# Kernel tuning notes

Hardware: AMD Instinct MI355X
Metric: run time of the kernel (lower is better)

## Reference

```python
import jax, jax.numpy as jnp
import numpy as np
import math

B, T, D, H, E = 4, 2048, 1024, 4096, 8
CAPACITY_FACTOR = 1.0
MIN_CAPACITY = 4
Z_LOSS_COEF = 0.001
AUX_LOSS_COEF = 0.01


def setup_inputs() -> dict:
    key = jax.random.key(0)
    ks = jax.random.split(key, 5)
    x = jax.random.normal(ks[0], (B, T, D), jnp.float32)
    Wg = jax.random.normal(ks[1], (D, E), jnp.float32) * 0.02
    W1 = jax.random.normal(ks[2], (E, D, H), jnp.float32) * (1.0 / math.sqrt(D))
    b1 = jnp.zeros((E, H), jnp.float32)
    W2 = jax.random.normal(ks[3], (E, H, D), jnp.float32) * (1.0 / math.sqrt(H))
    b2 = jnp.zeros((E, D), jnp.float32)
    return {"x": x, "Wg": Wg, "W1": W1, "b1": b1, "W2": W2, "b2": b2}


def reference(x, Wg, W1, b1, W2, b2):
    b, t, d = x.shape
    e = Wg.shape[1]
    N = b * t
    capacity = max(MIN_CAPACITY, math.ceil(CAPACITY_FACTOR * N / e))  # static
    xf = x.reshape(N, d)

    # ---- Router (top-1, z-loss + aux load-balancing loss) ----
    logits = xf @ Wg                                   # [N, E]
    probs = jax.nn.softmax(logits, axis=-1)
    z_loss = jnp.mean(jax.nn.logsumexp(logits, axis=-1) ** 2)
    expert_index = jnp.argmax(logits, axis=-1)         # [N]
    expert_prob = jnp.take_along_axis(probs, expert_index[:, None], axis=1)[:, 0]
    counts = jax.ops.segment_sum(jnp.ones((N,), jnp.float32), expert_index,
                                 num_segments=e)       # bincount
    f_i = counts / N
    p_i = probs.mean(axis=0)
    aux_loss = AUX_LOSS_COEF * e * jnp.sum(f_i * p_i) + Z_LOSS_COEF * z_loss

    # ---- Sort-based dispatch ----
    sort_idx = jnp.argsort(expert_index)               # stable sort by expert
    se = expert_index[sort_idx]                        # sorted expert ids
    xs = xf[sort_idx]                                  # tokens in sorted order
    ps = expert_prob[sort_idx]                         # probs in sorted order
    counts_i = counts.astype(jnp.int32)
    start = jnp.cumsum(counts_i) - counts_i            # per-expert start offsets
    pos = jnp.arange(N, dtype=jnp.int32) - start[se]   # slot within expert
    keep = pos < capacity                              # capacity drop
    slot = jnp.where(keep, pos, capacity)              # overflow -> trash slot

    # Gather tokens into per-expert capacity buffer [E, capacity+1, D]
    buf = jnp.zeros((e, capacity + 1, d), xf.dtype).at[se, slot].set(xs)

    # ---- Batched per-expert MLP (grouped GEMM) ----
    h = jax.nn.gelu(jnp.einsum('ecd,edh->ech', buf, W1) + b1[:, None, :],
                    approximate=False)
    o = jnp.einsum('ech,ehd->ecd', h, W2) + b2[:, None, :]

    # ---- Combine: gather back, zero dropped tokens, unsort ----
    out_sorted = jnp.where(keep[:, None], o[se, slot], jnp.zeros((), o.dtype))
    out = jnp.zeros_like(xf).at[sort_idx].set(out_sorted)
    # NOTE: faithful to original code, which multiplies the UNSORTED output by
    # the SORTED probabilities (prob_sorted), a quirk of the source module.
    out = out * ps[:, None]
    return out.reshape(b, t, d), aux_loss
```

## Files before the change

kernel.cpp:

```cpp
#include <hip/hip_runtime.h>
#include <math.h>

#define N_TOK 8192
#define DIM   1024
#define NEXP  8
#define HID   4096
#define CAP   1024
#define TPT   (N_TOK / 256)
#define RT_BLOCKS 1024
#define RT_TPB 8

typedef _Float16 f16x8 __attribute__((ext_vector_type(8)));
typedef _Float16 f16x4 __attribute__((ext_vector_type(4)));
typedef float    f32x4 __attribute__((ext_vector_type(4)));

__device__ __forceinline__ float gelu_fast(float v) {
    const float v2 = v * v;
    const float u = v * (0.79788456f + 0.035677408136f * v2);
    const float ex = __expf(2.f * u);
    const float th = 1.f - 2.f / (1.f + ex);
    return 0.5f * v * (1.f + th);
}

__device__ __forceinline__ void gl_lds16(const void* g, void* l) {
    __builtin_amdgcn_global_load_lds(
        (const __attribute__((address_space(1))) unsigned int*)g,
        (__attribute__((address_space(3))) unsigned int*)l, 16, 0, 0);
}

__global__ __launch_bounds__(256) void router_kernel(
    const float* __restrict__ x, const float* __restrict__ Wg,
    int* __restrict__ ei, float* __restrict__ eprob,
    float* __restrict__ pp)
{
    __shared__ float psum_s[NEXP + 1];
    const int tid = threadIdx.x;
    const int w = tid >> 6, lane = tid & 63;
    if (tid <= NEXP) psum_s[tid] = 0.f;
    __syncthreads();

    float p_loc[NEXP];
#pragma unroll
    for (int e = 0; e < NEXP; ++e) p_loc[e] = 0.f;
    float z_loc = 0.f;

#pragma unroll
    for (int ti = 0; ti < 2; ++ti) {
        const int t = blockIdx.x * RT_TPB + w * 2 + ti;
        const float* xr = x + (size_t)t * DIM;
        float acc[NEXP];
#pragma unroll
        for (int e = 0; e < NEXP; ++e) acc[e] = 0.f;
#pragma unroll
        for (int k = 0; k < DIM / 256; ++k) {
            const int d = k * 256 + lane * 4;
            const float4 xv = *(const float4*)(xr + d);
            const float xs[4] = {xv.x, xv.y, xv.z, xv.w};
#pragma unroll
            for (int u = 0; u < 4; ++u) {
                const float4 w0 = *(const float4*)(Wg + (size_t)(d + u) * NEXP);
                const float4 w1 = *(const float4*)(Wg + (size_t)(d + u) * NEXP + 4);
                acc[0] += xs[u] * w0.x; acc[1] += xs[u] * w0.y;
                acc[2] += xs[u] * w0.z; acc[3] += xs[u] * w0.w;
                acc[4] += xs[u] * w1.x; acc[5] += xs[u] * w1.y;
                acc[6] += xs[u] * w1.z; acc[7] += xs[u] * w1.w;
            }
        }
#pragma unroll
        for (int off = 32; off > 0; off >>= 1) {
#pragma unroll
            for (int e = 0; e < NEXP; ++e)
                acc[e] += __shfl_down(acc[e], off, 64);
        }
        if (lane == 0) {
            float m = acc[0]; int arg = 0;
#pragma unroll
            for (int e = 1; e < NEXP; ++e) { if (acc[e] > m) { m = acc[e]; arg = e; } }
            float ex[NEXP]; float se = 0.f;
#pragma unroll
            for (int e = 0; e < NEXP; ++e) { ex[e] = expf(acc[e] - m); se += ex[e]; }
            const float lse = m + logf(se);
            const float inv = 1.f / se;
#pragma unroll
            for (int e = 0; e < NEXP; ++e) p_loc[e] += ex[e] * inv;
            z_loc += lse * lse;
            ei[t] = arg;
            eprob[t] = ex[arg] * inv;
        }
    }
    if (lane == 0) {
#pragma unroll
        for (int e = 0; e < NEXP; ++e) atomicAdd(&psum_s[e], p_loc[e]);
        atomicAdd(&psum_s[NEXP], z_loc);
    }
    __syncthreads();
    if (tid <= NEXP) pp[blockIdx.x * (NEXP + 1) + tid] = psum_s[tid];
}

__global__ __launch_bounds__(256) void dispatch_kernel(
    const int* __restrict__ ei, const float* __restrict__ eprob,
    int* __restrict__ slot_to_token, int* __restrict__ sort_idx,
    float* __restrict__ scale,
    const float* __restrict__ pp,
    int* __restrict__ dropped, int* __restrict__ n_dropped,
    float* __restrict__ aux_out)
{
    __shared__ int hist[NEXP][256];
    __shared__ int start_s[NEXP];
    __shared__ float red_s[4][NEXP + 1];
    __shared__ float tot_s[NEXP + 1];
    __shared__ int ndrop_s;
    const int t = threadIdx.x;
    const int w = t >> 6, lane = t & 63;
    if (t == 0) ndrop_s = 0;

    {
        float v[NEXP + 1];
#pragma unroll
        for (int j = 0; j <= NEXP; ++j) v[j] = 0.f;
        for (int g = 0; g < RT_BLOCKS / 256; ++g)
#pragma unroll
            for (int j = 0; j <= NEXP; ++j) v[j] += pp[(size_t)(g * 256 + t) * (NEXP + 1) + j];
#pragma unroll
        for (int j = 0; j <= NEXP; ++j) {
            float s = v[j];
#pragma unroll
            for (int off = 32; off > 0; off >>= 1) s += __shfl_down(s, off, 64);
            if (lane == 0) red_s[w][j] = s;
        }
    }
    __syncthreads();
    if (t <= NEXP) tot_s[t] = red_s[0][t] + red_s[1][t] + red_s[2][t] + red_s[3][t];
    __syncthreads();

    int le[TPT];
    int lh[NEXP];
#pragma unroll
    for (int e = 0; e < NEXP; ++e) lh[e] = 0;
    const int base = t * TPT;
    for (int i = 0; i < TPT; ++i) {
        const int e = ei[base + i];
        le[i] = e;
        lh[e]++;
    }
#pragma unroll
    for (int e = 0; e < NEXP; ++e) hist[e][t] = lh[e];
    __syncthreads();
    for (int off = 1; off < 256; off <<= 1) {
        int v[NEXP];
#pragma unroll
        for (int e = 0; e < NEXP; ++e) v[e] = (t >= off) ? hist[e][t - off] : 0;
        __syncthreads();
#pragma unroll
        for (int e = 0; e < NEXP; ++e) hist[e][t] += v[e];
        __syncthreads();
    }
    if (t == 0) {
        int s = 0;
        for (int e = 0; e < NEXP; ++e) { start_s[e] = s; s += hist[e][255]; }
    }
    __syncthreads();
    int run[NEXP];
#pragma unroll
    for (int e = 0; e < NEXP; ++e) run[e] = (t > 0) ? hist[e][t - 1] : 0;
    for (int i = 0; i < TPT; ++i) {
        const int n = base + i;
        const int e = le[i];
        const int pos = run[e]++;
        sort_idx[start_s[e] + pos] = n;
        if (pos < CAP) {
            slot_to_token[e * CAP + pos] = n;
        } else {
            const int di = atomicAdd(&ndrop_s, 1);
            dropped[di] = n;
        }
    }
    __syncthreads();
    for (int n = t; n < N_TOK; n += 256) scale[n] = eprob[sort_idx[n]];
    if (t == 0) {
        n_dropped[0] = ndrop_s;
        float s = 0.f;
        for (int e = 0; e < NEXP; ++e) {
            const float f = (float)hist[e][255] / (float)N_TOK;
            const float p = tot_s[e] / (float)N_TOK;
            s += f * p;
        }
        aux_out[0] = 0.01f * (float)NEXP * s + 0.001f * (tot_s[NEXP] / (float)N_TOK);
    }
}

__global__ __launch_bounds__(256) void zero_dropped_kernel(
    const int* __restrict__ dropped, const int* __restrict__ n_dropped,
    float* __restrict__ out)
{
    const int nd = n_dropped[0];
    const float4 z = make_float4(0.f, 0.f, 0.f, 0.f);
    for (int idx = blockIdx.x; idx < nd; idx += gridDim.x) {
        const int tok = dropped[idx];
        *(float4*)(out + (size_t)tok * DIM + threadIdx.x * 4) = z;
    }
}

__global__ __launch_bounds__(256) void gather_kernel(
    const float* __restrict__ x, const int* __restrict__ slot_to_token,
    _Float16* __restrict__ Xbuf)
{
    const int slot = blockIdx.x;
    const int tok = slot_to_token[slot];
    const int c = threadIdx.x * 4;
    float4 v = make_float4(0.f, 0.f, 0.f, 0.f);
    if (tok >= 0) v = *(const float4*)(x + (size_t)tok * DIM + c);
    f16x4 o;
    o[0] = (_Float16)v.x; o[1] = (_Float16)v.y;
    o[2] = (_Float16)v.z; o[3] = (_Float16)v.w;
    *(f16x4*)(Xbuf + (size_t)slot * DIM + c) = o;
}

template<int R, int C>
__global__ __launch_bounds__(256) void transpose_f32_f16(
    const float* __restrict__ in, _Float16* __restrict__ outT)
{
    const int e = blockIdx.z;
    const int r0 = blockIdx.y * 64, c0 = blockIdx.x * 64;
    const float* pin = in + (size_t)e * R * C;
    _Float16* pot = outT + (size_t)e * R * C;
    __shared__ _Float16 tile[64][72];
    const int tid = threadIdx.x;
    const int rr = tid >> 4, cc = (tid & 15) * 4;
#pragma unroll
    for (int ri = 0; ri < 4; ++ri) {
        const int row = rr + ri * 16;
        const float4 v = *(const float4*)&pin[(size_t)(r0 + row) * C + c0 + cc];
        tile[cc + 0][row] = (_Float16)v.x;
        tile[cc + 1][row] = (_Float16)v.y;
        tile[cc + 2][row] = (_Float16)v.z;
        tile[cc + 3][row] = (_Float16)v.w;
    }
    __syncthreads();
    const int c = tid >> 2, rs = (tid & 3) * 16;
    const f16x8 o0 = *(const f16x8*)&tile[c][rs];
    const f16x8 o1 = *(const f16x8*)&tile[c][rs + 8];
    _Float16* po = &pot[(size_t)(c0 + c) * R + r0 + rs];
    *(f16x8*)po = o0;
    *(f16x8*)(po + 8) = o1;
}

__global__ __launch_bounds__(256) void gemm1_kernel(
    const _Float16* __restrict__ A, const _Float16* __restrict__ Bt,
    const float* __restrict__ b1, _Float16* __restrict__ Hbuf)
{
    const int b = blockIdx.x;
    const int xcd = b & 7, q = b >> 3;
    const int nb = (xcd << 2) | (q & 3);
    const int mb = q >> 2;
    const int e  = mb >> 3;
    const _Float16* Ab = A  + (size_t)mb * 128 * DIM;
    const _Float16* Bb = Bt + (size_t)e * HID * DIM + (size_t)nb * 128 * DIM;
    __shared__ _Float16 As[128 * 32];
    __shared__ _Float16 Bs[128 * 32];
    const int tid = threadIdx.x;
    const int lane = tid & 63, w = tid >> 6;
    const int wm = (w >> 1) * 64, wn = (w & 1) * 64;
    const int lr = lane & 15, quad = lane >> 4;

    f32x4 acc[4][4];
#pragma unroll
    for (int i = 0; i < 4; ++i)
#pragma unroll
        for (int j = 0; j < 4; ++j) acc[i][j] = (f32x4)0.f;

    for (int k0 = 0; k0 < DIM; k0 += 32) {
#pragma unroll
        for (int i = 0; i < 2; ++i) {
            const int idx = i * 256 + tid;
            const int row = idx >> 2, s = idx & 3;
            const int seg = s ^ (row & 3);
            gl_lds16(Ab + (size_t)row * DIM + k0 + seg * 8, &As[idx * 8]);
            gl_lds16(Bb + (size_t)row * DIM + k0 + seg * 8, &Bs[idx * 8]);
        }
        __syncthreads();
        f16x8 af[4], bf[4];
#pragma unroll
        for (int i = 0; i < 4; ++i) {
            const int R = wm + i * 16 + lr;
            af[i] = *(const f16x8*)&As[R * 32 + (quad ^ (R & 3)) * 8];
        }
#pragma unroll
        for (int j = 0; j < 4; ++j) {
            const int R = wn + j * 16 + lr;
            bf[j] = *(const f16x8*)&Bs[R * 32 + (quad ^ (R & 3)) * 8];
        }
#pragma unroll
        for (int i = 0; i < 4; ++i)
#pragma unroll
            for (int j = 0; j < 4; ++j)
                acc[i][j] = __builtin_amdgcn_mfma_f32_16x16x32_f16(af[i], bf[j], acc[i][j], 0, 0, 0);
        __syncthreads();
    }
    float bias[4];
#pragma unroll
    for (int j = 0; j < 4; ++j)
        bias[j] = b1[(size_t)e * HID + (size_t)nb * 128 + wn + j * 16 + lr];
#pragma unroll
    for (int i = 0; i < 4; ++i) {
#pragma unroll
        for (int r = 0; r < 4; ++r) {
            const size_t row = (size_t)mb * 128 + wm + i * 16 + quad * 4 + r;
            _Float16* hr = Hbuf + row * HID + (size_t)nb * 128;
#pragma unroll
            for (int j = 0; j < 4; ++j)
                hr[wn + j * 16 + lr] = (_Float16)gelu_fast(acc[i][j][r] + bias[j]);
        }
    }
}

__global__ __launch_bounds__(256) void gemm2_kernel(
    const _Float16* __restrict__ A, const _Float16* __restrict__ Bt,
    const float* __restrict__ b2, const int* __restrict__ slot_to_token,
    const float* __restrict__ scale, float* __restrict__ out)
{
    const int mb = blockIdx.x;
    const int nb = blockIdx.y;
    const int e  = mb >> 3;
    const _Float16* Ab = A  + (size_t)mb * 128 * HID;
    const _Float16* Bb = Bt + (size_t)e * DIM * HID + (size_t)nb * 128 * HID;
    __shared__ _Float16 As[128 * 32];
    __shared__ _Float16 Bs[128 * 32];
    const int tid = threadIdx.x;
    const int lane = tid & 63, w = tid >> 6;
    const int wm = (w >> 1) * 64, wn = (w & 1) * 64;
    const int lr = lane & 15, quad = lane >> 4;

    f32x4 acc[4][4];
#pragma unroll
    for (int i = 0; i < 4; ++i)
#pragma unroll
        for (int j = 0; j < 4; ++j) acc[i][j] = (f32x4)0.f;

    for (int k0 = 0; k0 < HID; k0 += 32) {
#pragma unroll
        for (int i = 0; i < 2; ++i) {
            const int idx = i * 256 + tid;
            const int row = idx >> 2, s = idx & 3;
            const int seg = s ^ (row & 3);
            gl_lds16(Ab + (size_t)row * HID + k0 + seg * 8, &As[idx * 8]);
            gl_lds16(Bb + (size_t)row * HID + k0 + seg * 8, &Bs[idx * 8]);
        }
        __syncthreads();
        f16x8 af[4], bf[4];
#pragma unroll
        for (int i = 0; i < 4; ++i) {
            const int R = wm + i * 16 + lr;
            af[i] = *(const f16x8*)&As[R * 32 + (quad ^ (R & 3)) * 8];
        }
#pragma unroll
        for (int j = 0; j < 4; ++j) {
            const int R = wn + j * 16 + lr;
            bf[j] = *(const f16x8*)&Bs[R * 32 + (quad ^ (R & 3)) * 8];
        }
#pragma unroll
        for (int i = 0; i < 4; ++i)
#pragma unroll
            for (int j = 0; j < 4; ++j)
                acc[i][j] = __builtin_amdgcn_mfma_f32_16x16x32_f16(af[i], bf[j], acc[i][j], 0, 0, 0);
        __syncthreads();
    }
    float bias[4];
#pragma unroll
    for (int j = 0; j < 4; ++j)
        bias[j] = b2[(size_t)e * DIM + (size_t)nb * 128 + wn + j * 16 + lr];
#pragma unroll
    for (int i = 0; i < 4; ++i) {
#pragma unroll
        for (int r = 0; r < 4; ++r) {
            const int slot = mb * 128 + wm + i * 16 + quad * 4 + r;
            const int tok = slot_to_token[slot];
            if (tok >= 0) {
                const float sc = scale[tok];
                float* orow = out + (size_t)tok * DIM + (size_t)nb * 128;
#pragma unroll
                for (int j = 0; j < 4; ++j)
                    orow[wn + j * 16 + lr] = (acc[i][j][r] + bias[j]) * sc;
            }
        }
    }
}

extern "C" void kernel_launch(void* const* d_in, const int* in_sizes, int n_in,
                              void* d_out, int out_size, void* d_ws, size_t ws_size,
                              hipStream_t stream)
{
    const float* x  = (const float*)d_in[0];
    const float* Wg = (const float*)d_in[1];
    const float* W1 = (const float*)d_in[2];
    const float* b1 = (const float*)d_in[3];
    const float* W2 = (const float*)d_in[4];
    const float* b2 = (const float*)d_in[5];
    float* out = (float*)d_out;

    _Float16* Wt   = (_Float16*)d_ws;
    _Float16* Xbuf = Wt + (size_t)NEXP * HID * DIM;
    _Float16* Hbuf = Xbuf + (size_t)N_TOK * DIM;
    int*   ei    = (int*)(Hbuf + (size_t)N_TOK * HID);
    float* eprob = (float*)(ei + N_TOK);
    int*   sort_idx = (int*)(eprob + N_TOK);
    float* scale = (float*)(sort_idx + N_TOK);
    int*   s2t   = (int*)(scale + N_TOK);
    float* pp    = (float*)(s2t + NEXP * CAP);
    int*   dropped = (int*)(pp + RT_BLOCKS * (NEXP + 1));
    int*   n_dropped = dropped + N_TOK;

    hipMemsetAsync(s2t, 0xFF, (size_t)NEXP * CAP * sizeof(int), stream);

    transpose_f32_f16<DIM, HID><<<dim3(HID / 64, DIM / 64, NEXP), 256, 0, stream>>>(W1, Wt);
    router_kernel<<<RT_BLOCKS, 256, 0, stream>>>(x, Wg, ei, eprob, pp);
    dispatch_kernel<<<1, 256, 0, stream>>>(ei, eprob, s2t, sort_idx, scale,
                                           pp, dropped, n_dropped,
                                           out + (size_t)N_TOK * DIM);
    zero_dropped_kernel<<<128, 256, 0, stream>>>(dropped, n_dropped, out);
    gather_kernel<<<NEXP * CAP, 256, 0, stream>>>(x, s2t, Xbuf);
    gemm1_kernel<<<2048, 256, 0, stream>>>(Xbuf, Wt, b1, Hbuf);
    transpose_f32_f16<HID, DIM><<<dim3(DIM / 64, HID / 64, NEXP), 256, 0, stream>>>(W2, Wt);
    gemm2_kernel<<<dim3(64, 8), 256, 0, stream>>>(Hbuf, Wt, b2, s2t, scale, out);
}
```

Baseline: 590.0 us.

## Triple-buffer MoE grouped GEMMs with 256x128 tiles and XCD-aware expert mapping

```diff
diff --git a/kernel.cpp b/kernel.cpp
--- a/kernel.cpp
+++ b/kernel.cpp
@@ -245,142 +245,215 @@
     *(f16x8*)(po + 8) = o1;
 }
 
-__global__ __launch_bounds__(256) void gemm1_kernel(
+
+__global__ __launch_bounds__(256, 2) void gemm1_kernel(
     const _Float16* __restrict__ A, const _Float16* __restrict__ Bt,
     const float* __restrict__ b1, _Float16* __restrict__ Hbuf)
 {
     const int b = blockIdx.x;
     const int xcd = b & 7, q = b >> 3;
-    const int nb = (xcd << 2) | (q & 3);
-    const int mb = q >> 2;
-    const int e  = mb >> 3;
-    const _Float16* Ab = A  + (size_t)mb * 128 * DIM;
+    const int mbl = q & 3, nb = q >> 2;
+    const int e = xcd, mb = (xcd << 2) | mbl;
+    const _Float16* Ab = A  + (size_t)mb * 256 * DIM;
     const _Float16* Bb = Bt + (size_t)e * HID * DIM + (size_t)nb * 128 * DIM;
-    __shared__ _Float16 As[128 * 32];
-    __shared__ _Float16 Bs[128 * 32];
+    __shared__ _Float16 As[3][256 * 32];
+    __shared__ _Float16 Bs[3][128 * 32];
     const int tid = threadIdx.x;
     const int lane = tid & 63, w = tid >> 6;
-    const int wm = (w >> 1) * 64, wn = (w & 1) * 64;
+    const int wr = w >> 1, wc = w & 1;
     const int lr = lane & 15, quad = lane >> 4;
-
-    f32x4 acc[4][4];
-#pragma unroll
-    for (int i = 0; i < 4; ++i)
-#pragma unroll
-        for (int j = 0; j < 4; ++j) acc[i][j] = (f32x4)0.f;
-
-    for (int k0 = 0; k0 < DIM; k0 += 32) {
+    const int rb = wr * 128, cb = wc * 64;
+
+    auto stage = [&](int t, int buf) {
+#pragma unroll
+        for (int i = 0; i < 4; ++i) {
+            const int idx = i * 256 + tid;
+            const int row = idx >> 2, s = idx & 3;
+            const int seg = s ^ ((row >> 1) & 3);
+            gl_lds16(Ab + (size_t)row * DIM + t * 32 + seg * 8, &As[buf][idx * 8]);
+        }
 #pragma unroll
         for (int i = 0; i < 2; ++i) {
             const int idx = i * 256 + tid;
             const int row = idx >> 2, s = idx & 3;
-            const int seg = s ^ (row & 3);
-            gl_lds16(Ab + (size_t)row * DIM + k0 + seg * 8, &As[idx * 8]);
-            gl_lds16(Bb + (size_t)row * DIM + k0 + seg * 8, &Bs[idx * 8]);
-        }
-        __syncthreads();
-        f16x8 af[4], bf[4];
-#pragma unroll
-        for (int i = 0; i < 4; ++i) {
-            const int R = wm + i * 16 + lr;
-            af[i] = *(const f16x8*)&As[R * 32 + (quad ^ (R & 3)) * 8];
-        }
-#pragma unroll
-        for (int j = 0; j < 4; ++j) {
-            const int R = wn + j * 16 + lr;
-            bf[j] = *(const f16x8*)&Bs[R * 32 + (quad ^ (R & 3)) * 8];
-        }
-#pragma unroll
-        for (int i = 0; i < 4; ++i)
-#pragma unroll
-            for (int j = 0; j < 4; ++j)
-                acc[i][j] = __builtin_amdgcn_mfma_f32_16x16x32_f16(af[i], bf[j], acc[i][j], 0, 0, 0);
-        __syncthreads();
-    }
+            const int seg = s ^ ((row >> 1) & 3);
+            gl_lds16(Bb + (size_t)row * DIM + t * 32 + seg * 8, &Bs[buf][idx * 8]);
+        }
+    };
+
+    f32x4 acc[8][4];
+#pragma unroll
+    for (int i = 0; i < 8; ++i)
+#pragma unroll
+        for (int j = 0; j < 4; ++j) acc[i][j] = (f32x4)0.f;
+
+    stage(0, 0);
+    stage(1, 1);
+    const int NT = DIM / 32;
+    int cur = 0;
+    for (int t = 0; t < NT; ++t) {
+        asm volatile("s_waitcnt vmcnt(6)" ::: "memory");
+        __builtin_amdgcn_s_barrier();
+        if (t + 2 < NT) {
+            int nx = cur + 2; if (nx >= 3) nx -= 3;
+            stage(t + 2, nx);
+        }
+        f16x8 af[8], bf[4];
+#pragma unroll
+        for (int m = 0; m < 4; ++m) {
+            const int R = rb + m * 16 + lr;
+            af[m] = *(const f16x8*)&As[cur][R * 32 + (quad ^ ((R >> 1) & 3)) * 8];
+        }
+#pragma unroll
+        for (int n = 0; n < 4; ++n) {
+            const int R = cb + n * 16 + lr;
+            bf[n] = *(const f16x8*)&Bs[cur][R * 32 + (quad ^ ((R >> 1) & 3)) * 8];
+        }
+        __builtin_amdgcn_s_barrier();
+        __builtin_amdgcn_s_setprio(1);
+#pragma unroll
+        for (int m = 0; m < 4; ++m)
+#pragma unroll
+            for (int n = 0; n < 4; ++n)
+                acc[m][n] = __builtin_amdgcn_mfma_f32_16x16x32_f16(af[m], bf[n], acc[m][n], 0, 0, 0);
+        __builtin_amdgcn_s_setprio(0);
+#pragma unroll
+        for (int m = 4; m < 8; ++m) {
+            const int R = rb + m * 16 + lr;
+            af[m] = *(const f16x8*)&As[cur][R * 32 + (quad ^ ((R >> 1) & 3)) * 8];
+        }
+        __builtin_amdgcn_s_setprio(1);
+#pragma unroll
+        for (int m = 4; m < 8; ++m)
+#pragma unroll
+            for (int n = 0; n < 4; ++n)
+                acc[m][n] = __builtin_amdgcn_mfma_f32_16x16x32_f16(af[m], bf[n], acc[m][n], 0, 0, 0);
+        __builtin_amdgcn_s_setprio(0);
+        cur = cur + 1; if (cur >= 3) cur -= 3;
+    }
+
+    const int colb = nb * 128 + cb;
     float bias[4];
 #pragma unroll
-    for (int j = 0; j < 4; ++j)
-        bias[j] = b1[(size_t)e * HID + (size_t)nb * 128 + wn + j * 16 + lr];
-#pragma unroll
-    for (int i = 0; i < 4; ++i) {
+    for (int n = 0; n < 4; ++n)
+        bias[n] = b1[(size_t)e * HID + colb + n * 16 + lr];
+#pragma unroll
+    for (int m = 0; m < 8; ++m) {
 #pragma unroll
         for (int r = 0; r < 4; ++r) {
-            const size_t row = (size_t)mb * 128 + wm + i * 16 + quad * 4 + r;
-            _Float16* hr = Hbuf + row * HID + (size_t)nb * 128;
-#pragma unroll
-            for (int j = 0; j < 4; ++j)
-                hr[wn + j * 16 + lr] = (_Float16)gelu_fast(acc[i][j][r] + bias[j]);
-        }
-    }
-}
-
-__global__ __launch_bounds__(256) void gemm2_kernel(
+            const size_t row = (size_t)mb * 256 + rb + m * 16 + quad * 4 + r;
+            _Float16* hr = Hbuf + row * HID + colb;
+#pragma unroll
+            for (int n = 0; n < 4; ++n)
+                hr[n * 16 + lr] = (_Float16)gelu_fast(acc[m][n][r] + bias[n]);
+        }
+    }
+}
+
+__global__ __launch_bounds__(256, 2) void gemm2_kernel(
     const _Float16* __restrict__ A, const _Float16* __restrict__ Bt,
     const float* __restrict__ b2, const int* __restrict__ slot_to_token,
     const float* __restrict__ scale, float* __restrict__ out)
 {
-    const int mb = blockIdx.x;
-    const int nb = blockIdx.y;
-    const int e  = mb >> 3;
-    const _Float16* Ab = A  + (size_t)mb * 128 * HID;
+    const int b = blockIdx.x;
+    const int xcd = b & 7, q = b >> 3;
+    const int mbl = q >> 3, nb = q & 7;
+    const int e = xcd, mb = (xcd << 2) | mbl;
+    const _Float16* Ab = A  + (size_t)mb * 256 * HID;
     const _Float16* Bb = Bt + (size_t)e * DIM * HID + (size_t)nb * 128 * HID;
-    __shared__ _Float16 As[128 * 32];
-    __shared__ _Float16 Bs[128 * 32];
+    __shared__ _Float16 As[3][256 * 32];
+    __shared__ _Float16 Bs[3][128 * 32];
     const int tid = threadIdx.x;
     const int lane = tid & 63, w = tid >> 6;
-    const int wm = (w >> 1) * 64, wn = (w & 1) * 64;
+    const int wr = w >> 1, wc = w & 1;
     const int lr = lane & 15, quad = lane >> 4;
-
-    f32x4 acc[4][4];
-#pragma unroll
-    for (int i = 0; i < 4; ++i)
-#pragma unroll
-        for (int j = 0; j < 4; ++j) acc[i][j] = (f32x4)0.f;
-
-    for (int k0 = 0; k0 < HID; k0 += 32) {
+    const int rb = wr * 128, cb = wc * 64;
+
+    auto stage = [&](int t, int buf) {
+#pragma unroll
+        for (int i = 0; i < 4; ++i) {
+            const int idx = i * 256 + tid;
+            const int row = idx >> 2, s = idx & 3;
+            const int seg = s ^ ((row >> 1) & 3);
+            gl_lds16(Ab + (size_t)row * HID + t * 32 + seg * 8, &As[buf][idx * 8]);
+        }
 #pragma unroll
         for (int i = 0; i < 2; ++i) {
             const int idx = i * 256 + tid;
             const int row = idx >> 2, s = idx & 3;
-            const int seg = s ^ (row & 3);
-            gl_lds16(Ab + (size_t)row * HID + k0 + seg * 8, &As[idx * 8]);
-            gl_lds16(Bb + (size_t)row * HID + k0 + seg * 8, &Bs[idx * 8]);
-        }
-        __syncthreads();
-        f16x8 af[4], bf[4];
-#pragma unroll
-        for (int i = 0; i < 4; ++i) {
-            const int R = wm + i * 16 + lr;
-            af[i] = *(const f16x8*)&As[R * 32 + (quad ^ (R & 3)) * 8];
-        }
-#pragma unroll
-        for (int j = 0; j < 4; ++j) {
-            const int R = wn + j * 16 + lr;
-            bf[j] = *(const f16x8*)&Bs[R * 32 + (quad ^ (R & 3)) * 8];
-        }
-#pragma unroll
-        for (int i = 0; i < 4; ++i)
-#pragma unroll
-            for (int j = 0; j < 4; ++j)
-                acc[i][j] = __builtin_amdgcn_mfma_f32_16x16x32_f16(af[i], bf[j], acc[i][j], 0, 0, 0);
-        __syncthreads();
-    }
+            const int seg = s ^ ((row >> 1) & 3);
+            gl_lds16(Bb + (size_t)row * HID + t * 32 + seg * 8, &Bs[buf][idx * 8]);
+        }
+    };
+
+    f32x4 acc[8][4];
+#pragma unroll
+    for (int i = 0; i < 8; ++i)
+#pragma unroll
+        for (int j = 0; j < 4; ++j) acc[i][j] = (f32x4)0.f;
+
+    stage(0, 0);
+    stage(1, 1);
+    const int NT = HID / 32;
+    int cur = 0;
+    for (int t = 0; t < NT; ++t) {
+        asm volatile("s_waitcnt vmcnt(6)" ::: "memory");
+        __builtin_amdgcn_s_barrier();
+        if (t + 2 < NT) {
+            int nx = cur + 2; if (nx >= 3) nx -= 3;
+            stage(t + 2, nx);
+        }
+        f16x8 af[8], bf[4];
+#pragma unroll
+        for (int m = 0; m < 4; ++m) {
+            const int R = rb + m * 16 + lr;
+            af[m] = *(const f16x8*)&As[cur][R * 32 + (quad ^ ((R >> 1) & 3)) * 8];
+        }
+#pragma unroll
+        for (int n = 0; n < 4; ++n) {
+            const int R = cb + n * 16 + lr;
+            bf[n] = *(const f16x8*)&Bs[cur][R * 32 + (quad ^ ((R >> 1) & 3)) * 8];
+        }
+        __builtin_amdgcn_s_barrier();
+        __builtin_amdgcn_s_setprio(1);
+#pragma unroll
+        for (int m = 0; m < 4; ++m)
+#pragma unroll
+            for (int n = 0; n < 4; ++n)
+                acc[m][n] = __builtin_amdgcn_mfma_f32_16x16x32_f16(af[m], bf[n], acc[m][n], 0, 0, 0);
+        __builtin_amdgcn_s_setprio(0);
+#pragma unroll
+        for (int m = 4; m < 8; ++m) {
+            const int R = rb + m * 16 + lr;
+            af[m] = *(const f16x8*)&As[cur][R * 32 + (quad ^ ((R >> 1) & 3)) * 8];
+        }
+        __builtin_amdgcn_s_setprio(1);
+#pragma unroll
+        for (int m = 4; m < 8; ++m)
+#pragma unroll
+            for (int n = 0; n < 4; ++n)
+                acc[m][n] = __builtin_amdgcn_mfma_f32_16x16x32_f16(af[m], bf[n], acc[m][n], 0, 0, 0);
+        __builtin_amdgcn_s_setprio(0);
+        cur = cur + 1; if (cur >= 3) cur -= 3;
+    }
+
+    const int colb = nb * 128 + cb;
     float bias[4];
 #pragma unroll
-    for (int j = 0; j < 4; ++j)
-        bias[j] = b2[(size_t)e * DIM + (size_t)nb * 128 + wn + j * 16 + lr];
-#pragma unroll
-    for (int i = 0; i < 4; ++i) {
+    for (int n = 0; n < 4; ++n)
+        bias[n] = b2[(size_t)e * DIM + colb + n * 16 + lr];
+#pragma unroll
+    for (int m = 0; m < 8; ++m) {
 #pragma unroll
         for (int r = 0; r < 4; ++r) {
-            const int slot = mb * 128 + wm + i * 16 + quad * 4 + r;
+            const int slot = mb * 256 + rb + m * 16 + quad * 4 + r;
             const int tok = slot_to_token[slot];
             if (tok >= 0) {
                 const float sc = scale[tok];
-                float* orow = out + (size_t)tok * DIM + (size_t)nb * 128;
-#pragma unroll
-                for (int j = 0; j < 4; ++j)
-                    orow[wn + j * 16 + lr] = (acc[i][j][r] + bias[j]) * sc;
+                float* orow = out + (size_t)tok * DIM + colb;
+#pragma unroll
+                for (int n = 0; n < 4; ++n)
+                    orow[n * 16 + lr] = (acc[m][n][r] + bias[n]) * sc;
             }
         }
     }
@@ -419,7 +492,7 @@
                                            out + (size_t)N_TOK * DIM);
     zero_dropped_kernel<<<128, 256, 0, stream>>>(dropped, n_dropped, out);
     gather_kernel<<<NEXP * CAP, 256, 0, stream>>>(x, s2t, Xbuf);
-    gemm1_kernel<<<2048, 256, 0, stream>>>(Xbuf, Wt, b1, Hbuf);
+    gemm1_kernel<<<1024, 256, 0, stream>>>(Xbuf, Wt, b1, Hbuf);
     transpose_f32_f16<HID, DIM><<<dim3(DIM / 64, HID / 64, NEXP), 256, 0, stream>>>(W2, Wt);
-    gemm2_kernel<<<dim3(64, 8), 256, 0, stream>>>(Hbuf, Wt, b2, s2t, scale, out);
-}
+    gemm2_kernel<<<256, 256, 0, stream>>>(Hbuf, Wt, b2, s2t, scale, out);
+}
```

Result: slower. 618.1 us (+4.8%).
